# Kernel optimization log

Hardware: AMD Instinct MI355X
Metric: run time of the kernel (lower is better)

The kernel has to match this reference:

```python
import jax, jax.numpy as jnp
import numpy as np

H = 768


def _glorot(key, shape):
    fan_in = shape[-1]
    return jax.random.normal(key, shape, dtype=jnp.float32) / np.sqrt(fan_in)


def setup_inputs() -> dict:
    key = jax.random.key(0)
    ks = jax.random.split(key, 12)
    B, L, K, Lg = 8, 256, 32, 128
    return {
        "x": jax.random.normal(ks[0], (B, L, H), dtype=jnp.float32),
        "s": jax.random.normal(ks[1], (B, K, H), dtype=jnp.float32),
        "g": jax.random.normal(ks[2], (B, Lg, H), dtype=jnp.float32),
        "Wq": _glorot(ks[3], (H, H)),
        "bq": jnp.zeros((H,), jnp.float32),
        "Wkv": _glorot(ks[4], (2 * H, H)),
        "bkv": jnp.zeros((2 * H,), jnp.float32),
        "Wg1": _glorot(ks[5], (H, 2 * H)),
        "bg1": jnp.zeros((H,), jnp.float32),
        "Wg2": _glorot(ks[6], (H, 2 * H)),
        "bg2": jnp.zeros((H,), jnp.float32),
    }


def _gate(xb, yb, W, b):
    # gate = sigmoid(Linear(concat([x, y], -1))) using split-weight trick:
    # concat([x,y]) @ W.T = x @ Wx.T + y @ Wy.T  (avoids materializing 2H concat)
    Wx, Wy = W[:, :H], W[:, H:]
    gate = jax.nn.sigmoid(jnp.einsum('blkh,oh->blko', xb, Wx)
                          + jnp.einsum('blkh,oh->blko', yb, Wy) + b)
    return gate * xb + (1.0 - gate) * yb


def reference(x, s, g, Wq, bq, Wkv, bkv, Wg1, bg1, Wg2, bg2):
    B, L, _ = x.shape
    K = s.shape[1]
    q = jnp.einsum('blh,oh->blo', x, Wq) + bq                    # (B,L,H)
    kv = jnp.einsum('bmh,oh->bmo', g, Wkv) + bkv                 # (B,Lg,2H)
    k, v = kv[..., :H], kv[..., H:]
    scores = jnp.einsum('blh,bmh->blm', q, k) / np.sqrt(H)       # (B,L,Lg)
    scores = jax.nn.softmax(scores, axis=-1)
    gctx = jnp.einsum('blm,bmh->blh', scores, v)                 # (B,L,H)
    # broadcast to (B,L,K,H)
    gb = jnp.broadcast_to(gctx[:, :, None, :], (B, L, K, H))
    hb = jnp.broadcast_to(x[:, :, None, :], (B, L, K, H))
    sb = jnp.broadcast_to(s[:, None, :, :], (B, L, K, H))
    h = _gate(hb, gb, Wg1, bg1)
    h = _gate(h, sb, Wg2, bg2)
    return h
```

## Files before the change

### kernel.cpp

```cpp
#include <hip/hip_runtime.h>
#include <math.h>

#define Hd 768
#define Bb 8
#define Ll 256
#define Kk 32
#define LG 128

using half4 = __attribute__((ext_vector_type(4))) _Float16;
using half8 = __attribute__((ext_vector_type(8))) _Float16;
using f32x4 = __attribute__((ext_vector_type(4))) float;

__device__ __forceinline__ float sigm(float z) { return 1.f / (1.f + __expf(-z)); }

struct ConvArgs {
    const float* src[8];
    _Float16*    dst[8];
    int cum[9];
    int sstr[8];
    int dstr[8];
    int rl[8];
};

__global__ __launch_bounds__(256) void conv_multi(ConvArgs a) {
    int c = blockIdx.x * 256 + threadIdx.x;
    if (c >= a.cum[8]) return;
    int s = 0;
    while (c >= a.cum[s + 1]) ++s;
    const int lc  = c - a.cum[s];
    const unsigned cpr = (unsigned)(a.rl[s] >> 3);
    const unsigned row = (unsigned)lc / cpr;
    const int col = (lc - (int)(row * cpr)) * 8;
    const float* sp = a.src[s] + (size_t)row * a.sstr[s] + col;
    float4 v0 = *(const float4*)sp;
    float4 v1 = *(const float4*)(sp + 4);
    half8 h;
    h[0] = (_Float16)v0.x; h[1] = (_Float16)v0.y; h[2] = (_Float16)v0.z; h[3] = (_Float16)v0.w;
    h[4] = (_Float16)v1.x; h[5] = (_Float16)v1.y; h[6] = (_Float16)v1.z; h[7] = (_Float16)v1.w;
    *(half8*)(a.dst[s] + (size_t)row * a.dstr[s] + col) = h;
}

__global__ __launch_bounds__(256) void gemm_f16(
    const _Float16* __restrict__ A, int lda, long sA,
    const _Float16* __restrict__ W, int ldw, long sW,
    const float* __restrict__ bias,
    float* __restrict__ C, int ldc, long sC,
    _Float16* __restrict__ C2, int ldc2, long sC2,
    int Kd, int kvsplit,
    _Float16* __restrict__ K16, _Float16* __restrict__ VT16)
{
    __shared__ _Float16 As[128][72];
    __shared__ _Float16 Ws[64][72];

    const int t    = threadIdx.x;
    const int w    = t >> 6;
    const int lane = t & 63;
    const int quad = lane >> 4;
    const int l16  = lane & 15;
    const int bm   = blockIdx.y * 128;
    const int bn   = blockIdx.x * 64;
    const int z    = blockIdx.z;
    A += (size_t)z * sA;
    W += (size_t)z * sW;

    const int sr = t >> 3;
    const int sk = (t & 7) * 8;

    f32x4 acc[2][4] = {};

    for (int k0 = 0; k0 < Kd; k0 += 64) {
        half8 av[4], wv[2];
        #pragma unroll
        for (int i = 0; i < 4; ++i)
            av[i] = *(const half8*)(A + (size_t)(bm + i * 32 + sr) * lda + k0 + sk);
        #pragma unroll
        for (int i = 0; i < 2; ++i)
            wv[i] = *(const half8*)(W + (size_t)(bn + i * 32 + sr) * ldw + k0 + sk);
        __syncthreads();
        #pragma unroll
        for (int i = 0; i < 4; ++i) *(half8*)&As[i * 32 + sr][sk] = av[i];
        #pragma unroll
        for (int i = 0; i < 2; ++i) *(half8*)&Ws[i * 32 + sr][sk] = wv[i];
        __syncthreads();
        #pragma unroll
        for (int kk = 0; kk < 2; ++kk) {
            half8 af[2], bf[4];
            af[0] = *(const half8*)&As[w * 32 + l16][kk * 32 + quad * 8];
            af[1] = *(const half8*)&As[w * 32 + 16 + l16][kk * 32 + quad * 8];
            #pragma unroll
            for (int j = 0; j < 4; ++j)
                bf[j] = *(const half8*)&Ws[j * 16 + l16][kk * 32 + quad * 8];
            #pragma unroll
            for (int rt = 0; rt < 2; ++rt)
                #pragma unroll
                for (int j = 0; j < 4; ++j)
                    acc[rt][j] = __builtin_amdgcn_mfma_f32_16x16x32_f16(
                        af[rt], bf[j], acc[rt][j], 0, 0, 0);
        }
    }

    #pragma unroll
    for (int rt = 0; rt < 2; ++rt) {
        #pragma unroll
        for (int j = 0; j < 4; ++j) {
            const int col  = bn + j * 16 + l16;
            const int row0 = bm + w * 32 + rt * 16 + quad * 4;
            const float bv = bias ? bias[col] : 0.f;
            if (kvsplit) {
                if (col < 768) {
                    #pragma unroll
                    for (int r = 0; r < 4; ++r)
                        K16[(size_t)(row0 + r) * 768 + col] = (_Float16)(acc[rt][j][r] + bv);
                } else {
                    const int b = row0 >> 7, h = col - 768, m0 = row0 & 127;
                    half4 hv;
                    #pragma unroll
                    for (int r = 0; r < 4; ++r) hv[r] = (_Float16)(acc[rt][j][r] + bv);
                    *(half4*)(VT16 + ((size_t)(b * 768 + h)) * 128 + m0) = hv;
                }
            } else {
                #pragma unroll
                for (int r = 0; r < 4; ++r) {
                    const float v = acc[rt][j][r] + bv;
                    const size_t rr = (size_t)(row0 + r);
                    if (C)  C[(size_t)z * sC + rr * ldc + col] = v;
                    if (C2) C2[(size_t)z * sC2 + rr * ldc2 + col] = (_Float16)v;
                }
            }
        }
    }
}

struct G3Desc {
    const _Float16* A;
    const _Float16* W;
    const float* bias;
    void* o0;
    void* o1;
    int lda, ldw, mode, nbx;
};
struct G3Args { G3Desc d[3]; int cum[4]; };

__global__ __launch_bounds__(256) void gemm3(G3Args ga) {
    __shared__ _Float16 As[128][72];
    __shared__ _Float16 Ws[64][72];

    const int t    = threadIdx.x;
    const int w    = t >> 6;
    const int lane = t & 63;
    const int quad = lane >> 4;
    const int l16  = lane & 15;

    int s = 0;
    const int bid = blockIdx.x;
    while (bid >= ga.cum[s + 1]) ++s;
    const int local = bid - ga.cum[s];
    const int nbx   = ga.d[s].nbx;
    const int by    = local / nbx;
    const int bx    = local - by * nbx;
    const int bm    = by * 128;
    const int bn    = bx * 64;
    const _Float16* A = ga.d[s].A;
    const _Float16* W = ga.d[s].W;
    const int lda = ga.d[s].lda;
    const int ldw = ga.d[s].ldw;

    const int sr = t >> 3;
    const int sk = (t & 7) * 8;

    f32x4 acc[2][4] = {};

    for (int k0 = 0; k0 < 768; k0 += 64) {
        half8 av[4], wv[2];
        #pragma unroll
        for (int i = 0; i < 4; ++i)
            av[i] = *(const half8*)(A + (size_t)(bm + i * 32 + sr) * lda + k0 + sk);
        #pragma unroll
        for (int i = 0; i < 2; ++i)
            wv[i] = *(const half8*)(W + (size_t)(bn + i * 32 + sr) * ldw + k0 + sk);
        __syncthreads();
        #pragma unroll
        for (int i = 0; i < 4; ++i) *(half8*)&As[i * 32 + sr][sk] = av[i];
        #pragma unroll
        for (int i = 0; i < 2; ++i) *(half8*)&Ws[i * 32 + sr][sk] = wv[i];
        __syncthreads();
        #pragma unroll
        for (int kk = 0; kk < 2; ++kk) {
            half8 af[2], bf[4];
            af[0] = *(const half8*)&As[w * 32 + l16][kk * 32 + quad * 8];
            af[1] = *(const half8*)&As[w * 32 + 16 + l16][kk * 32 + quad * 8];
            #pragma unroll
            for (int j = 0; j < 4; ++j)
                bf[j] = *(const half8*)&Ws[j * 16 + l16][kk * 32 + quad * 8];
            #pragma unroll
            for (int rt = 0; rt < 2; ++rt)
                #pragma unroll
                for (int j = 0; j < 4; ++j)
                    acc[rt][j] = __builtin_amdgcn_mfma_f32_16x16x32_f16(
                        af[rt], bf[j], acc[rt][j], 0, 0, 0);
        }
    }

    const int mode = ga.d[s].mode;
    const float* bias = ga.d[s].bias;
    #pragma unroll
    for (int rt = 0; rt < 2; ++rt) {
        #pragma unroll
        for (int j = 0; j < 4; ++j) {
            const int col  = bn + j * 16 + l16;
            const int row0 = bm + w * 32 + rt * 16 + quad * 4;
            const float bv = bias ? bias[col] : 0.f;
            if (mode == 0) {
                _Float16* C2 = (_Float16*)ga.d[s].o0;
                #pragma unroll
                for (int r = 0; r < 4; ++r)
                    C2[(size_t)(row0 + r) * 768 + col] = (_Float16)(acc[rt][j][r] + bv);
            } else if (mode == 1) {
                _Float16* K16  = (_Float16*)ga.d[s].o0;
                _Float16* VT16 = (_Float16*)ga.d[s].o1;
                if (col < 768) {
                    #pragma unroll
                    for (int r = 0; r < 4; ++r)
                        K16[(size_t)(row0 + r) * 768 + col] = (_Float16)(acc[rt][j][r] + bv);
                } else {
                    const int b = row0 >> 7, h = col - 768, m0 = row0 & 127;
                    half4 hv;
                    #pragma unroll
                    for (int r = 0; r < 4; ++r) hv[r] = (_Float16)(acc[rt][j][r] + bv);
                    *(half4*)(VT16 + ((size_t)(b * 768 + h)) * 128 + m0) = hv;
                }
            } else {
                float* C = (float*)ga.d[s].o0;
                #pragma unroll
                for (int r = 0; r < 4; ++r)
                    C[(size_t)(row0 + r) * 768 + col] = acc[rt][j][r] + bv;
            }
        }
    }
}

__global__ __launch_bounds__(256) void attn_scores_sm(
    const _Float16* __restrict__ Q, const _Float16* __restrict__ Kt,
    _Float16* __restrict__ P)
{
    __shared__ _Float16 As[64][72];
    __shared__ _Float16 Ws[128][72];

    const int t    = threadIdx.x;
    const int w    = t >> 6;
    const int lane = t & 63;
    const int quad = lane >> 4;
    const int l16  = lane & 15;
    const int z    = blockIdx.y;
    const int bm   = blockIdx.x * 64;
    const _Float16* A = Q  + (size_t)z * 256 * 768 + (size_t)bm * 768;
    const _Float16* W = Kt + (size_t)z * 128 * 768;

    const int sr = t >> 3;
    const int sk = (t & 7) * 8;

    f32x4 acc[8] = {};

    for (int k0 = 0; k0 < 768; k0 += 64) {
        half8 av[2], wv[4];
        #pragma unroll
        for (int i = 0; i < 2; ++i)
            av[i] = *(const half8*)(A + (size_t)(i * 32 + sr) * 768 + k0 + sk);
        #pragma unroll
        for (int i = 0; i < 4; ++i)
            wv[i] = *(const half8*)(W + (size_t)(i * 32 + sr) * 768 + k0 + sk);
        __syncthreads();
        #pragma unroll
        for (int i = 0; i < 2; ++i) *(half8*)&As[i * 32 + sr][sk] = av[i];
        #pragma unroll
        for (int i = 0; i < 4; ++i) *(half8*)&Ws[i * 32 + sr][sk] = wv[i];
        __syncthreads();
        #pragma unroll
        for (int kk = 0; kk < 2; ++kk) {
            half8 af = *(const half8*)&As[w * 16 + l16][kk * 32 + quad * 8];
            #pragma unroll
            for (int j = 0; j < 8; ++j) {
                half8 bf = *(const half8*)&Ws[j * 16 + l16][kk * 32 + quad * 8];
                acc[j] = __builtin_amdgcn_mfma_f32_16x16x32_f16(af, bf, acc[j], 0, 0, 0);
            }
        }
    }

    const float scale = 0.03608439182435161f;
    #pragma unroll
    for (int r = 0; r < 4; ++r) {
        float v[8];
        float mx = -1e30f;
        #pragma unroll
        for (int j = 0; j < 8; ++j) { v[j] = acc[j][r] * scale; mx = fmaxf(mx, v[j]); }
        #pragma unroll
        for (int off = 8; off; off >>= 1) mx = fmaxf(mx, __shfl_xor(mx, off, 16));
        float sum = 0.f;
        #pragma unroll
        for (int j = 0; j < 8; ++j) { v[j] = __expf(v[j] - mx); sum += v[j]; }
        #pragma unroll
        for (int off = 8; off; off >>= 1) sum += __shfl_xor(sum, off, 16);
        const float inv = 1.f / sum;
        const int row = bm + w * 16 + quad * 4 + r;
        _Float16* Pr = P + (size_t)z * 256 * 128 + (size_t)row * 128;
        #pragma unroll
        for (int j = 0; j < 8; ++j) Pr[j * 16 + l16] = (_Float16)(v[j] * inv);
    }
}

__global__ __launch_bounds__(256) void gemm_gate1(
    const _Float16* __restrict__ A,
    const _Float16* __restrict__ W,
    const float* __restrict__ bias,
    const float* __restrict__ X,
    const float* __restrict__ GC,
    float* __restrict__ H1,
    _Float16* __restrict__ H16)
{
    __shared__ _Float16 As[128][72];
    __shared__ _Float16 Ws[64][72];

    const int t    = threadIdx.x;
    const int w    = t >> 6;
    const int lane = t & 63;
    const int quad = lane >> 4;
    const int l16  = lane & 15;
    const int bm   = blockIdx.y * 128;
    const int bn   = blockIdx.x * 64;

    const int sr = t >> 3;
    const int sk = (t & 7) * 8;

    f32x4 acc[2][4] = {};

    for (int k0 = 0; k0 < 1536; k0 += 64) {
        half8 av[4], wv[2];
        #pragma unroll
        for (int i = 0; i < 4; ++i)
            av[i] = *(const half8*)(A + (size_t)(bm + i * 32 + sr) * 1536 + k0 + sk);
        #pragma unroll
        for (int i = 0; i < 2; ++i)
            wv[i] = *(const half8*)(W + (size_t)(bn + i * 32 + sr) * 1536 + k0 + sk);
        __syncthreads();
        #pragma unroll
        for (int i = 0; i < 4; ++i) *(half8*)&As[i * 32 + sr][sk] = av[i];
        #pragma unroll
        for (int i = 0; i < 2; ++i) *(half8*)&Ws[i * 32 + sr][sk] = wv[i];
        __syncthreads();
        #pragma unroll
        for (int kk = 0; kk < 2; ++kk) {
            half8 af[2], bf[4];
            af[0] = *(const half8*)&As[w * 32 + l16][kk * 32 + quad * 8];
            af[1] = *(const half8*)&As[w * 32 + 16 + l16][kk * 32 + quad * 8];
            #pragma unroll
            for (int j = 0; j < 4; ++j)
                bf[j] = *(const half8*)&Ws[j * 16 + l16][kk * 32 + quad * 8];
            #pragma unroll
            for (int rt = 0; rt < 2; ++rt)
                #pragma unroll
                for (int j = 0; j < 4; ++j)
                    acc[rt][j] = __builtin_amdgcn_mfma_f32_16x16x32_f16(
                        af[rt], bf[j], acc[rt][j], 0, 0, 0);
        }
    }

    #pragma unroll
    for (int rt = 0; rt < 2; ++rt) {
        #pragma unroll
        for (int j = 0; j < 4; ++j) {
            const int col  = bn + j * 16 + l16;
            const int row0 = bm + w * 32 + rt * 16 + quad * 4;
            const float bv = bias[col];
            #pragma unroll
            for (int r = 0; r < 4; ++r) {
                const size_t off = (size_t)(row0 + r) * 768 + col;
                const float g = sigm(acc[rt][j][r] + bv);
                const float o = g * X[off] + (1.f - g) * GC[off];
                H1[off]  = o;
                H16[off] = (_Float16)o;
            }
        }
    }
}

__global__ __launch_bounds__(256) void gemm_final(
    const _Float16* __restrict__ A,
    const _Float16* __restrict__ W,
    const float* __restrict__ bias,
    const float* __restrict__ Ebuf,
    const float* __restrict__ Sbuf,
    const float* __restrict__ H1,
    float* __restrict__ out)
{
    __shared__ union {
        struct { _Float16 As[128][72]; _Float16 Ws[64][72]; } a;
        float Ds[128][76];
    } u;
    __shared__ float Es[32][64];
    __shared__ float Ss[32][64];

    const int t    = threadIdx.x;
    const int w    = t >> 6;
    const int lane = t & 63;
    const int quad = lane >> 4;
    const int l16  = lane & 15;
    const int bm   = blockIdx.y * 128;
    const int bn   = blockIdx.x * 64;
    const int bK   = (bm >> 8) * 32;

    const int sr = t >> 3;
    const int sk = (t & 7) * 8;

    #pragma unroll
    for (int i = 0; i < 2; ++i) {
        const int idx = t + i * 256;
        const int k = idx >> 4, c = (idx & 15) * 4;
        *(float4*)&Es[k][c] = *(const float4*)(Ebuf + (size_t)(bK + k) * 768 + bn + c);
        *(float4*)&Ss[k][c] = *(const float4*)(Sbuf + (size_t)(bK + k) * 768 + bn + c);
    }

    f32x4 acc[2][4] = {};

    for (int k0 = 0; k0 < 768; k0 += 64) {
        half8 av[4], wv[2];
        #pragma unroll
        for (int i = 0; i < 4; ++i)
            av[i] = *(const half8*)(A + (size_t)(bm + i * 32 + sr) * 768 + k0 + sk);
        #pragma unroll
        for (int i = 0; i < 2; ++i)
            wv[i] = *(const half8*)(W + (size_t)(bn + i * 32 + sr) * 768 + k0 + sk);
        __syncthreads();
        #pragma unroll
        for (int i = 0; i < 4; ++i) *(half8*)&u.a.As[i * 32 + sr][sk] = av[i];
        #pragma unroll
        for (int i = 0; i < 2; ++i) *(half8*)&u.a.Ws[i * 32 + sr][sk] = wv[i];
        __syncthreads();
        #pragma unroll
        for (int kk = 0; kk < 2; ++kk) {
            half8 af[2], bf[4];
            af[0] = *(const half8*)&u.a.As[w * 32 + l16][kk * 32 + quad * 8];
            af[1] = *(const half8*)&u.a.As[w * 32 + 16 + l16][kk * 32 + quad * 8];
            #pragma unroll
            for (int j = 0; j < 4; ++j)
                bf[j] = *(const half8*)&u.a.Ws[j * 16 + l16][kk * 32 + quad * 8];
            #pragma unroll
            for (int rt = 0; rt < 2; ++rt)
                #pragma unroll
                for (int j = 0; j < 4; ++j)
                    acc[rt][j] = __builtin_amdgcn_mfma_f32_16x16x32_f16(
                        af[rt], bf[j], acc[rt][j], 0, 0, 0);
        }
    }

    __syncthreads();
    #pragma unroll
    for (int rt = 0; rt < 2; ++rt) {
        #pragma unroll
        for (int j = 0; j < 4; ++j) {
            const int col = j * 16 + l16;
            const float bv = bias[bn + col];
            #pragma unroll
            for (int r = 0; r < 4; ++r)
                u.Ds[w * 32 + rt * 16 + quad * 4 + r][col] = acc[rt][j][r] + bv;
        }
    }
    __syncthreads();

    const int c  = (t & 15) * 4;
    const int r0 = (t >> 4) * 8;
    float4 d[8], h[8];
    #pragma unroll
    for (int rr = 0; rr < 8; ++rr) {
        d[rr] = *(const float4*)&u.Ds[r0 + rr][c];
        h[rr] = *(const float4*)(H1 + (size_t)(bm + r0 + rr) * 768 + bn + c);
    }
    float* ob = out + (size_t)(bm + r0) * 32 * 768 + bn + c;
    for (int k = 0; k < 32; ++k) {
        const float4 e  = *(const float4*)&Es[k][c];
        const float4 sv = *(const float4*)&Ss[k][c];
        #pragma unroll
        for (int rr = 0; rr < 8; ++rr) {
            float4 o; float g;
            g = sigm(d[rr].x + e.x); o.x = g * h[rr].x + (1.f - g) * sv.x;
            g = sigm(d[rr].y + e.y); o.y = g * h[rr].y + (1.f - g) * sv.y;
            g = sigm(d[rr].z + e.z); o.z = g * h[rr].z + (1.f - g) * sv.z;
            g = sigm(d[rr].w + e.w); o.w = g * h[rr].w + (1.f - g) * sv.w;
            *(float4*)(ob + (size_t)(rr * 32 + k) * 768) = o;
        }
    }
}

extern "C" void kernel_launch(void* const* d_in, const int* in_sizes, int n_in,
                              void* d_out, int out_size, void* d_ws, size_t ws_size,
                              hipStream_t stream) {
    const float* x   = (const float*)d_in[0];
    const float* s   = (const float*)d_in[1];
    const float* g   = (const float*)d_in[2];
    const float* Wq  = (const float*)d_in[3];
    const float* bq  = (const float*)d_in[4];
    const float* Wkv = (const float*)d_in[5];
    const float* bkv = (const float*)d_in[6];
    const float* Wg1 = (const float*)d_in[7];
    const float* bg1 = (const float*)d_in[8];
    const float* Wg2 = (const float*)d_in[9];
    const float* bg2 = (const float*)d_in[10];

    char* w = (char*)d_ws;
    _Float16* P16    = (_Float16*)(w + 0);
    _Float16* xg16   = (_Float16*)(w + 524288);
    _Float16* g16    = (_Float16*)(w + 6815744);
    _Float16* s16    = (_Float16*)(w + 8388608);
    _Float16* q16    = (_Float16*)(w + 8781824);
    _Float16* k16    = (_Float16*)(w + 11927552);
    _Float16* vT16   = (_Float16*)(w + 13500416);
    _Float16* Wq16   = (_Float16*)(w + 15073280);
    _Float16* Wkv16  = (_Float16*)(w + 16252928);
    _Float16* Wg116  = (_Float16*)(w + 18612224);
    _Float16* Wg2a16 = (_Float16*)(w + 20971520);
    _Float16* Wg2b16 = (_Float16*)(w + 22151168);
    float*    bufE   = (float*)(w + 23330816);
    float*    bufC   = (float*)(w + 24117248);
    float*    bufB   = (float*)(w + 30408704);
    _Float16* h116   = (_Float16*)(w + 36700160);
    float* out = (float*)d_out;

    const dim3 blk(256);

    ConvArgs ca;
    ca.src[0] = x;         ca.dst[0] = xg16;   ca.sstr[0] = 768;  ca.dstr[0] = 1536; ca.rl[0] = 768;
    ca.src[1] = g;         ca.dst[1] = g16;    ca.sstr[1] = 768;  ca.dstr[1] = 768;  ca.rl[1] = 768;
    ca.src[2] = s;         ca.dst[2] = s16;    ca.sstr[2] = 768;  ca.dstr[2] = 768;  ca.rl[2] = 768;
    ca.src[3] = Wq;        ca.dst[3] = Wq16;   ca.sstr[3] = 768;  ca.dstr[3] = 768;  ca.rl[3] = 768;
    ca.src[4] = Wkv;       ca.dst[4] = Wkv16;  ca.sstr[4] = 768;  ca.dstr[4] = 768;  ca.rl[4] = 768;
    ca.src[5] = Wg1;       ca.dst[5] = Wg116;  ca.sstr[5] = 1536; ca.dstr[5] = 1536; ca.rl[5] = 1536;
    ca.src[6] = Wg2;       ca.dst[6] = Wg2a16; ca.sstr[6] = 1536; ca.dstr[6] = 768;  ca.rl[6] = 768;
    ca.src[7] = Wg2 + 768; ca.dst[7] = Wg2b16; ca.sstr[7] = 1536; ca.dstr[7] = 768;  ca.rl[7] = 768;
    ca.cum[0] = 0;      ca.cum[1] = 196608; ca.cum[2] = 294912; ca.cum[3] = 319488;
    ca.cum[4] = 393216; ca.cum[5] = 540672; ca.cum[6] = 688128; ca.cum[7] = 761856;
    ca.cum[8] = 835584;
    conv_multi<<<dim3(3264), blk, 0, stream>>>(ca);

    G3Args ga = {};
    ga.d[0] = { xg16, Wq16,   bq,      (void*)q16,  nullptr,     1536, 768, 0, 12 };
    ga.d[1] = { g16,  Wkv16,  bkv,     (void*)k16,  (void*)vT16, 768,  768, 1, 24 };
    ga.d[2] = { s16,  Wg2b16, nullptr, (void*)bufE, nullptr,     768,  768, 2, 12 };
    ga.cum[0] = 0; ga.cum[1] = 192; ga.cum[2] = 384; ga.cum[3] = 408;
    gemm3<<<dim3(408), blk, 0, stream>>>(ga);

    attn_scores_sm<<<dim3(4, 8), blk, 0, stream>>>(q16, k16, P16);

    gemm_f16<<<dim3(12, 2, 8), blk, 0, stream>>>(
        P16, 128, 256L * 128, vT16, 128, 768L * 128, nullptr,
        bufC, 768, 256L * 768, xg16 + 768, 1536, 256L * 1536, 128, 0, nullptr, nullptr);

    gemm_gate1<<<dim3(12, 16), blk, 0, stream>>>(
        xg16, Wg116, bg1, x, bufC, bufB, h116);

    gemm_final<<<dim3(12, 16), blk, 0, stream>>>(
        h116, Wg2a16, bg2, bufE, s, bufB, out);
}
```

Baseline: 322.3 us.

## Prefetch next K-tile into registers during MFMA compute in all GEMM kernels

```diff
diff --git a/kernel.cpp b/kernel.cpp
--- a/kernel.cpp
+++ b/kernel.cpp
@@ -68,20 +68,30 @@
 
     f32x4 acc[2][4] = {};
 
+    half8 av[4], wv[2];
+    #pragma unroll
+    for (int i = 0; i < 4; ++i)
+        av[i] = *(const half8*)(A + (size_t)(bm + i * 32 + sr) * lda + sk);
+    #pragma unroll
+    for (int i = 0; i < 2; ++i)
+        wv[i] = *(const half8*)(W + (size_t)(bn + i * 32 + sr) * ldw + sk);
+
     for (int k0 = 0; k0 < Kd; k0 += 64) {
-        half8 av[4], wv[2];
-        #pragma unroll
-        for (int i = 0; i < 4; ++i)
-            av[i] = *(const half8*)(A + (size_t)(bm + i * 32 + sr) * lda + k0 + sk);
-        #pragma unroll
-        for (int i = 0; i < 2; ++i)
-            wv[i] = *(const half8*)(W + (size_t)(bn + i * 32 + sr) * ldw + k0 + sk);
         __syncthreads();
         #pragma unroll
         for (int i = 0; i < 4; ++i) *(half8*)&As[i * 32 + sr][sk] = av[i];
         #pragma unroll
         for (int i = 0; i < 2; ++i) *(half8*)&Ws[i * 32 + sr][sk] = wv[i];
         __syncthreads();
+        if (k0 + 64 < Kd) {
+            #pragma unroll
+            for (int i = 0; i < 4; ++i)
+                av[i] = *(const half8*)(A + (size_t)(bm + i * 32 + sr) * lda + k0 + 64 + sk);
+            #pragma unroll
+            for (int i = 0; i < 2; ++i)
+                wv[i] = *(const half8*)(W + (size_t)(bn + i * 32 + sr) * ldw + k0 + 64 + sk);
+        }
+        __builtin_amdgcn_sched_barrier(0);
         #pragma unroll
         for (int kk = 0; kk < 2; ++kk) {
             half8 af[2], bf[4];
@@ -170,20 +180,30 @@
 
     f32x4 acc[2][4] = {};
 
+    half8 av[4], wv[2];
+    #pragma unroll
+    for (int i = 0; i < 4; ++i)
+        av[i] = *(const half8*)(A + (size_t)(bm + i * 32 + sr) * lda + sk);
+    #pragma unroll
+    for (int i = 0; i < 2; ++i)
+        wv[i] = *(const half8*)(W + (size_t)(bn + i * 32 + sr) * ldw + sk);
+
     for (int k0 = 0; k0 < 768; k0 += 64) {
-        half8 av[4], wv[2];
-        #pragma unroll
-        for (int i = 0; i < 4; ++i)
-            av[i] = *(const half8*)(A + (size_t)(bm + i * 32 + sr) * lda + k0 + sk);
-        #pragma unroll
-        for (int i = 0; i < 2; ++i)
-            wv[i] = *(const half8*)(W + (size_t)(bn + i * 32 + sr) * ldw + k0 + sk);
         __syncthreads();
         #pragma unroll
         for (int i = 0; i < 4; ++i) *(half8*)&As[i * 32 + sr][sk] = av[i];
         #pragma unroll
         for (int i = 0; i < 2; ++i) *(half8*)&Ws[i * 32 + sr][sk] = wv[i];
         __syncthreads();
+        if (k0 + 64 < 768) {
+            #pragma unroll
+            for (int i = 0; i < 4; ++i)
+                av[i] = *(const half8*)(A + (size_t)(bm + i * 32 + sr) * lda + k0 + 64 + sk);
+            #pragma unroll
+            for (int i = 0; i < 2; ++i)
+                wv[i] = *(const half8*)(W + (size_t)(bn + i * 32 + sr) * ldw + k0 + 64 + sk);
+        }
+        __builtin_amdgcn_sched_barrier(0);
         #pragma unroll
         for (int kk = 0; kk < 2; ++kk) {
             half8 af[2], bf[4];
@@ -261,20 +281,30 @@
 
     f32x4 acc[8] = {};
 
+    half8 av[2], wv[4];
+    #pragma unroll
+    for (int i = 0; i < 2; ++i)
+        av[i] = *(const half8*)(A + (size_t)(i * 32 + sr) * 768 + sk);
+    #pragma unroll
+    for (int i = 0; i < 4; ++i)
+        wv[i] = *(const half8*)(W + (size_t)(i * 32 + sr) * 768 + sk);
+
     for (int k0 = 0; k0 < 768; k0 += 64) {
-        half8 av[2], wv[4];
-        #pragma unroll
-        for (int i = 0; i < 2; ++i)
-            av[i] = *(const half8*)(A + (size_t)(i * 32 + sr) * 768 + k0 + sk);
-        #pragma unroll
-        for (int i = 0; i < 4; ++i)
-            wv[i] = *(const half8*)(W + (size_t)(i * 32 + sr) * 768 + k0 + sk);
         __syncthreads();
         #pragma unroll
         for (int i = 0; i < 2; ++i) *(half8*)&As[i * 32 + sr][sk] = av[i];
         #pragma unroll
         for (int i = 0; i < 4; ++i) *(half8*)&Ws[i * 32 + sr][sk] = wv[i];
         __syncthreads();
+        if (k0 + 64 < 768) {
+            #pragma unroll
+            for (int i = 0; i < 2; ++i)
+                av[i] = *(const half8*)(A + (size_t)(i * 32 + sr) * 768 + k0 + 64 + sk);
+            #pragma unroll
+            for (int i = 0; i < 4; ++i)
+                wv[i] = *(const half8*)(W + (size_t)(i * 32 + sr) * 768 + k0 + 64 + sk);
+        }
+        __builtin_amdgcn_sched_barrier(0);
         #pragma unroll
         for (int kk = 0; kk < 2; ++kk) {
             half8 af = *(const half8*)&As[w * 16 + l16][kk * 32 + quad * 8];
@@ -333,20 +363,30 @@
 
     f32x4 acc[2][4] = {};
 
+    half8 av[4], wv[2];
+    #pragma unroll
+    for (int i = 0; i < 4; ++i)
+        av[i] = *(const half8*)(A + (size_t)(bm + i * 32 + sr) * 1536 + sk);
+    #pragma unroll
+    for (int i = 0; i < 2; ++i)
+        wv[i] = *(const half8*)(W + (size_t)(bn + i * 32 + sr) * 1536 + sk);
+
     for (int k0 = 0; k0 < 1536; k0 += 64) {
-        half8 av[4], wv[2];
-        #pragma unroll
-        for (int i = 0; i < 4; ++i)
-            av[i] = *(const half8*)(A + (size_t)(bm + i * 32 + sr) * 1536 + k0 + sk);
-        #pragma unroll
-        for (int i = 0; i < 2; ++i)
-            wv[i] = *(const half8*)(W + (size_t)(bn + i * 32 + sr) * 1536 + k0 + sk);
         __syncthreads();
         #pragma unroll
         for (int i = 0; i < 4; ++i) *(half8*)&As[i * 32 + sr][sk] = av[i];
         #pragma unroll
         for (int i = 0; i < 2; ++i) *(half8*)&Ws[i * 32 + sr][sk] = wv[i];
         __syncthreads();
+        if (k0 + 64 < 1536) {
+            #pragma unroll
+            for (int i = 0; i < 4; ++i)
+                av[i] = *(const half8*)(A + (size_t)(bm + i * 32 + sr) * 1536 + k0 + 64 + sk);
+            #pragma unroll
+            for (int i = 0; i < 2; ++i)
+                wv[i] = *(const half8*)(W + (size_t)(bn + i * 32 + sr) * 1536 + k0 + 64 + sk);
+        }
+        __builtin_amdgcn_sched_barrier(0);
         #pragma unroll
         for (int kk = 0; kk < 2; ++kk) {
             half8 af[2], bf[4];
@@ -421,20 +461,30 @@
 
     f32x4 acc[2][4] = {};
 
+    half8 av[4], wv[2];
+    #pragma unroll
+    for (int i = 0; i < 4; ++i)
+        av[i] = *(const half8*)(A + (size_t)(bm + i * 32 + sr) * 768 + sk);
+    #pragma unroll
+    for (int i = 0; i < 2; ++i)
+        wv[i] = *(const half8*)(W + (size_t)(bn + i * 32 + sr) * 768 + sk);
+
     for (int k0 = 0; k0 < 768; k0 += 64) {
-        half8 av[4], wv[2];
-        #pragma unroll
-        for (int i = 0; i < 4; ++i)
-            av[i] = *(const half8*)(A + (size_t)(bm + i * 32 + sr) * 768 + k0 + sk);
-        #pragma unroll
-        for (int i = 0; i < 2; ++i)
-            wv[i] = *(const half8*)(W + (size_t)(bn + i * 32 + sr) * 768 + k0 + sk);
         __syncthreads();
         #pragma unroll
         for (int i = 0; i < 4; ++i) *(half8*)&u.a.As[i * 32 + sr][sk] = av[i];
         #pragma unroll
         for (int i = 0; i < 2; ++i) *(half8*)&u.a.Ws[i * 32 + sr][sk] = wv[i];
         __syncthreads();
+        if (k0 + 64 < 768) {
+            #pragma unroll
+            for (int i = 0; i < 4; ++i)
+                av[i] = *(const half8*)(A + (size_t)(bm + i * 32 + sr) * 768 + k0 + 64 + sk);
+            #pragma unroll
+            for (int i = 0; i < 2; ++i)
+                wv[i] = *(const half8*)(W + (size_t)(bn + i * 32 + sr) * 768 + k0 + 64 + sk);
+        }
+        __builtin_amdgcn_sched_barrier(0);
         #pragma unroll
         for (int kk = 0; kk < 2; ++kk) {
             half8 af[2], bf[4];
```

Result: faster. 314.1 us (-2.5%).
